# Performance work log

Hardware: AMD Instinct MI355X
Metric: run time of the kernel (lower is better)

## Reference

```python
import jax, jax.numpy as jnp
import numpy as np

GAMMA = 1.0

def setup_inputs() -> dict:
    key = jax.random.key(0)
    kx, ky = jax.random.split(key)
    X = jax.random.normal(kx, (8192, 64), dtype=jnp.float32)
    Y = jax.random.normal(ky, (8192, 64), dtype=jnp.float32)
    return {"X": X, "Y": Y}

def reference(X, Y):
    x2 = jnp.sum(X * X, axis=-1)            # (n,)
    y2 = jnp.sum(Y * Y, axis=-1)            # (m,)
    xy = X @ Y.T                            # (n, m)
    dist2 = x2[:, None] + y2[None, :] - 2.0 * xy
    dist2 = jnp.maximum(dist2, 0.0)         # numerical guard
    return jnp.exp(-GAMMA * dist2)
```

## Files before the change

### kernel.cpp

```cpp
#include <hip/hip_runtime.h>

typedef __attribute__((ext_vector_type(8))) short          short8_t;
typedef __attribute__((ext_vector_type(8))) unsigned short ushort8_t;
typedef __attribute__((ext_vector_type(4))) float          floatx4;

constexpr int N_ROWS = 8192;
constexpr int DIM    = 64;
constexpr int PANEL  = 128 * DIM;

__device__ __forceinline__ unsigned short bf16_rne(float f) {
    unsigned int u = __float_as_uint(f);
    u += 0x7FFFu + ((u >> 16) & 1u);
    return (unsigned short)(u >> 16);
}

__global__ void __launch_bounds__(256)
split_norms_kernel(const float* __restrict__ X, const float* __restrict__ Y,
                   float* __restrict__ x2n, float* __restrict__ y2n,
                   unsigned short* __restrict__ Xs, unsigned short* __restrict__ Ys) {
    const int t  = blockIdx.x * 256 + threadIdx.x;
    const int r  = t >> 1;
    const int h  = t & 1;
    const int p  = r >> 7;
    const int rl = r & 127;
    const int g  = rl >> 4;
    const int li = rl & 15;
    const size_t pb = (size_t)p * (2 * PANEL);

    const float4* xr = reinterpret_cast<const float4*>(X + (size_t)r * DIM + h * 32);
    const float4* yr = reinterpret_cast<const float4*>(Y + (size_t)r * DIM + h * 32);

    float sx = 0.f, sy = 0.f;
#pragma unroll
    for (int c = 0; c < 4; ++c) {
        const int off = ((g * 2 + h) * 64 + c * 16 + li) * 8;
        float f[8];
        ushort8_t hi, lo;

        *reinterpret_cast<float4*>(&f[0]) = xr[2 * c];
        *reinterpret_cast<float4*>(&f[4]) = xr[2 * c + 1];
#pragma unroll
        for (int e = 0; e < 8; ++e) {
            sx = fmaf(f[e], f[e], sx);
            unsigned short hh = bf16_rne(f[e]);
            hi[e] = hh;
            lo[e] = bf16_rne(f[e] - __uint_as_float((unsigned int)hh << 16));
        }
        *reinterpret_cast<ushort8_t*>(&Xs[pb + off])         = hi;
        *reinterpret_cast<ushort8_t*>(&Xs[pb + PANEL + off]) = lo;

        *reinterpret_cast<float4*>(&f[0]) = yr[2 * c];
        *reinterpret_cast<float4*>(&f[4]) = yr[2 * c + 1];
#pragma unroll
        for (int e = 0; e < 8; ++e) {
            sy = fmaf(f[e], f[e], sy);
            unsigned short hh = bf16_rne(f[e]);
            hi[e] = hh;
            lo[e] = bf16_rne(f[e] - __uint_as_float((unsigned int)hh << 16));
        }
        *reinterpret_cast<ushort8_t*>(&Ys[pb + off])         = hi;
        *reinterpret_cast<ushort8_t*>(&Ys[pb + PANEL + off]) = lo;
    }
    sx += __shfl_xor(sx, 1);
    sy += __shfl_xor(sy, 1);
    if (h == 0) { x2n[r] = -sx; y2n[r] = -sy; }
}

__global__ void __launch_bounds__(64)
rbf_mfma_kernel(const unsigned short* __restrict__ Xs,
                const unsigned short* __restrict__ Ys,
                const float* __restrict__ x2n, const float* __restrict__ y2n,
                float* __restrict__ out) {
    const int lane = threadIdx.x;
    const int row0 = blockIdx.y * 64;
    const int col0 = blockIdx.x * 64;
    const unsigned short* Xp = Xs + (size_t)(blockIdx.y >> 1) * (2 * PANEL);
    const unsigned short* Yp = Ys + (size_t)(blockIdx.x >> 1) * (2 * PANEL);
    const int gx0 = (blockIdx.y & 1) * 4;
    const int gy0 = (blockIdx.x & 1) * 4;

    floatx4 acc[4][4] = {};

#define GF(P, hl, g, ks)                                                       \
    (*reinterpret_cast<const short8_t*>(                                       \
        (P) + (hl) * PANEL + (((g) * 2 + (ks)) * 64 + lane) * 8))

#pragma unroll
    for (int ks = 0; ks < 2; ++ks) {
        short8_t aH[4], bH[4], aL[4], bL[4];
#pragma unroll
        for (int mi = 0; mi < 4; ++mi) aH[mi] = GF(Xp, 0, gx0 + mi, ks);
#pragma unroll
        for (int ni = 0; ni < 4; ++ni) bH[ni] = GF(Yp, 0, gy0 + ni, ks);
#pragma unroll
        for (int mi = 0; mi < 4; ++mi)
#pragma unroll
            for (int ni = 0; ni < 4; ++ni)
                acc[mi][ni] = __builtin_amdgcn_mfma_f32_16x16x32_bf16(
                    bH[ni], aH[mi], acc[mi][ni], 0, 0, 0);
#pragma unroll
        for (int ni = 0; ni < 4; ++ni) bL[ni] = GF(Yp, 1, gy0 + ni, ks);
#pragma unroll
        for (int mi = 0; mi < 4; ++mi)
#pragma unroll
            for (int ni = 0; ni < 4; ++ni)
                acc[mi][ni] = __builtin_amdgcn_mfma_f32_16x16x32_bf16(
                    bL[ni], aH[mi], acc[mi][ni], 0, 0, 0);
#pragma unroll
        for (int mi = 0; mi < 4; ++mi) aL[mi] = GF(Xp, 1, gx0 + mi, ks);
#pragma unroll
        for (int mi = 0; mi < 4; ++mi)
#pragma unroll
            for (int ni = 0; ni < 4; ++ni)
                acc[mi][ni] = __builtin_amdgcn_mfma_f32_16x16x32_bf16(
                    bH[ni], aL[mi], acc[mi][ni], 0, 0, 0);
    }
#undef GF

    const int li = lane & 15;
    const int lg = lane >> 4;
    const int orow = row0 + li;
    const int ocol = col0 + lg * 4;
#pragma unroll
    for (int mi = 0; mi < 4; ++mi) {
        const float xs = x2n[orow + mi * 16];
        float* obase = out + (size_t)(orow + mi * 16) * N_ROWS + ocol;
#pragma unroll
        for (int ni = 0; ni < 4; ++ni) {
            const float4 yv = *reinterpret_cast<const float4*>(&y2n[ocol + ni * 16]);
            floatx4 o;
            o[0] = __expf(fminf(fmaf(2.f, acc[mi][ni][0], xs + yv.x), 0.f));
            o[1] = __expf(fminf(fmaf(2.f, acc[mi][ni][1], xs + yv.y), 0.f));
            o[2] = __expf(fminf(fmaf(2.f, acc[mi][ni][2], xs + yv.z), 0.f));
            o[3] = __expf(fminf(fmaf(2.f, acc[mi][ni][3], xs + yv.w), 0.f));
            __builtin_nontemporal_store(o, reinterpret_cast<floatx4*>(obase + ni * 16));
        }
    }
}

extern "C" void kernel_launch(void* const* d_in, const int* in_sizes, int n_in,
                              void* d_out, int out_size, void* d_ws, size_t ws_size,
                              hipStream_t stream) {
    const float* X = (const float*)d_in[0];
    const float* Y = (const float*)d_in[1];
    float* out = (float*)d_out;

    float* x2n = (float*)d_ws;
    float* y2n = x2n + N_ROWS;
    unsigned short* Xs = (unsigned short*)(y2n + N_ROWS);
    unsigned short* Ys = Xs + (N_ROWS / 128) * 2 * PANEL;

    split_norms_kernel<<<(2 * N_ROWS) / 256, 256, 0, stream>>>(X, Y, x2n, y2n, Xs, Ys);

    dim3 grid(N_ROWS / 64, N_ROWS / 64);
    rbf_mfma_kernel<<<grid, 64, 0, stream>>>(Xs, Ys, x2n, y2n, out);
}
```

Measured before the change: 73.41 us.

## Stage Y strip in LDS via global_load_lds and keep X fragments in registers

Replaces the one-wave-per-64x64-tile grid with 256-thread blocks that each cover 256 rows by a 512-column strip. The strip's split-bf16 Y panels (128 KB) are copied into LDS once with direct global-to-LDS loads. Each wave keeps its X hi/lo fragments in registers and loops over eight 64-column chunks. This cuts redundant global operand loads and launch count, but the large LDS footprint limits occupancy to one block per CU and leaves little overlap between the initial LDS fill and compute.

```diff
diff --git a/kernel.cpp b/kernel.cpp
--- a/kernel.cpp
+++ b/kernel.cpp
@@ -7,11 +7,18 @@
 constexpr int N_ROWS = 8192;
 constexpr int DIM    = 64;
 constexpr int PANEL  = 128 * DIM;
+constexpr int STRIP  = 512;
 
 __device__ __forceinline__ unsigned short bf16_rne(float f) {
     unsigned int u = __float_as_uint(f);
     u += 0x7FFFu + ((u >> 16) & 1u);
     return (unsigned short)(u >> 16);
+}
+
+typedef __attribute__((address_space(1))) unsigned int gu32;
+typedef __attribute__((address_space(3))) unsigned int lu32;
+__device__ __forceinline__ void gload16(const void* g, void* l) {
+    __builtin_amdgcn_global_load_lds((gu32*)g, (lu32*)l, 16, 0, 0);
 }
 
 __global__ void __launch_bounds__(256)
@@ -66,74 +73,105 @@
     if (h == 0) { x2n[r] = -sx; y2n[r] = -sy; }
 }
 
-__global__ void __launch_bounds__(64)
+__global__ void __launch_bounds__(256)
 rbf_mfma_kernel(const unsigned short* __restrict__ Xs,
                 const unsigned short* __restrict__ Ys,
                 const float* __restrict__ x2n, const float* __restrict__ y2n,
                 float* __restrict__ out) {
-    const int lane = threadIdx.x;
-    const int row0 = blockIdx.y * 64;
-    const int col0 = blockIdx.x * 64;
-    const unsigned short* Xp = Xs + (size_t)(blockIdx.y >> 1) * (2 * PANEL);
-    const unsigned short* Yp = Ys + (size_t)(blockIdx.x >> 1) * (2 * PANEL);
-    const int gx0 = (blockIdx.y & 1) * 4;
-    const int gy0 = (blockIdx.x & 1) * 4;
+    extern __shared__ unsigned short Blds[];
 
-    floatx4 acc[4][4] = {};
+    const int tid  = threadIdx.x;
+    const int lane = tid & 63;
+    const int w    = tid >> 6;
+    const int strip = blockIdx.x;
+    const int band  = blockIdx.y;
 
-#define GF(P, hl, g, ks)                                                       \
-    (*reinterpret_cast<const short8_t*>(                                       \
-        (P) + (hl) * PANEL + (((g) * 2 + (ks)) * 64 + lane) * 8))
+    {
+        const unsigned short* src = Ys + (size_t)strip * (8 * PANEL);
+#pragma unroll
+        for (int it = 0; it < 32; ++it) {
+            const int ofs = ((w * 32 + it) * 64 + lane) * 8;
+            gload16(src + ofs, Blds + ofs);
+        }
+    }
 
+    const int row0 = band * 256 + w * 64;
+    short8_t aH[4][2], aL[4][2];
+    {
+        const int gx0 = row0 >> 4;
 #pragma unroll
-    for (int ks = 0; ks < 2; ++ks) {
-        short8_t aH[4], bH[4], aL[4], bL[4];
+        for (int gx = 0; gx < 4; ++gx) {
+            const int gabs = gx0 + gx;
+            const unsigned short* base = Xs + (size_t)(gabs >> 3) * (2 * PANEL);
+            const int g = gabs & 7;
 #pragma unroll
-        for (int mi = 0; mi < 4; ++mi) aH[mi] = GF(Xp, 0, gx0 + mi, ks);
-#pragma unroll
-        for (int ni = 0; ni < 4; ++ni) bH[ni] = GF(Yp, 0, gy0 + ni, ks);
-#pragma unroll
-        for (int mi = 0; mi < 4; ++mi)
-#pragma unroll
-            for (int ni = 0; ni < 4; ++ni)
-                acc[mi][ni] = __builtin_amdgcn_mfma_f32_16x16x32_bf16(
-                    bH[ni], aH[mi], acc[mi][ni], 0, 0, 0);
-#pragma unroll
-        for (int ni = 0; ni < 4; ++ni) bL[ni] = GF(Yp, 1, gy0 + ni, ks);
-#pragma unroll
-        for (int mi = 0; mi < 4; ++mi)
-#pragma unroll
-            for (int ni = 0; ni < 4; ++ni)
-                acc[mi][ni] = __builtin_amdgcn_mfma_f32_16x16x32_bf16(
-                    bL[ni], aH[mi], acc[mi][ni], 0, 0, 0);
-#pragma unroll
-        for (int mi = 0; mi < 4; ++mi) aL[mi] = GF(Xp, 1, gx0 + mi, ks);
-#pragma unroll
-        for (int mi = 0; mi < 4; ++mi)
-#pragma unroll
-            for (int ni = 0; ni < 4; ++ni)
-                acc[mi][ni] = __builtin_amdgcn_mfma_f32_16x16x32_bf16(
-                    bH[ni], aL[mi], acc[mi][ni], 0, 0, 0);
+            for (int ks = 0; ks < 2; ++ks) {
+                const int off = ((g * 2 + ks) * 64 + lane) * 8;
+                aH[gx][ks] = *reinterpret_cast<const short8_t*>(base + off);
+                aL[gx][ks] = *reinterpret_cast<const short8_t*>(base + PANEL + off);
+            }
+        }
     }
-#undef GF
+    __syncthreads();
 
     const int li = lane & 15;
     const int lg = lane >> 4;
-    const int orow = row0 + li;
-    const int ocol = col0 + lg * 4;
-#pragma unroll
-    for (int mi = 0; mi < 4; ++mi) {
-        const float xs = x2n[orow + mi * 16];
-        float* obase = out + (size_t)(orow + mi * 16) * N_ROWS + ocol;
+
+    for (int ch = 0; ch < 8; ++ch) {
+        short8_t bH[4][2], bL[4][2];
 #pragma unroll
         for (int ni = 0; ni < 4; ++ni) {
-            const float4 yv = *reinterpret_cast<const float4*>(&y2n[ocol + ni * 16]);
-            floatx4 o;
-            o[0] = __expf(fminf(fmaf(2.f, acc[mi][ni][0], xs + yv.x), 0.f));
-            o[1] = __expf(fminf(fmaf(2.f, acc[mi][ni][1], xs + yv.y), 0.f));
-            o[2] = __expf(fminf(fmaf(2.f, acc[mi][ni][2], xs + yv.z), 0.f));
-            o[3] = __expf(fminf(fmaf(2.f, acc[mi][ni][3], xs + yv.w), 0.f));
-            __builtin_nontemporal_store(o, reinterpret_cast<floatx4*>(obase + ni * 16));
+            const int gy = ch * 4 + ni;
+            const unsigned short* p =
+                Blds + (gy >> 3) * (2 * PANEL);
+            const int g = gy & 7;
+#pragma unroll
+            for (int ks = 0; ks < 2; ++ks) {
+                const int off = ((g * 2 + ks) * 64 + lane) * 8;
+                bH[ni][ks] = *reinterpret_cast<const short8_t*>(p + off);
+                bL[ni][ks] = *reinterpret_cast<const short8_t*>(p + PANEL + off);
+            }
+        }
+
+        floatx4 acc[4][4] = {};
+#pragma unroll
+        for (int ks = 0; ks < 2; ++ks) {
+#pragma unroll
+            for (int mi = 0; mi < 4; ++mi)
+#pragma unroll
+                for (int ni = 0; ni < 4; ++ni)
+                    acc[mi][ni] = __builtin_amdgcn_mfma_f32_16x16x32_bf16(
+                        bH[ni][ks], aH[mi][ks], acc[mi][ni], 0, 0, 0);
+#pragma unroll
+            for (int mi = 0; mi < 4; ++mi)
+#pragma unroll
+                for (int ni = 0; ni < 4; ++ni)
+                    acc[mi][ni] = __builtin_amdgcn_mfma_f32_16x16x32_bf16(
+                        bL[ni][ks], aH[mi][ks], acc[mi][ni], 0, 0, 0);
+#pragma unroll
+            for (int mi = 0; mi < 4; ++mi)
+#pragma unroll
+                for (int ni = 0; ni < 4; ++ni)
+                    acc[mi][ni] = __builtin_amdgcn_mfma_f32_16x16x32_bf16(
+                        bH[ni][ks], aL[mi][ks], acc[mi][ni], 0, 0, 0);
+        }
+
+        const int ocol = strip * STRIP + ch * 64 + lg * 4;
+#pragma unroll
+        for (int mi = 0; mi < 4; ++mi) {
+            const int rbase = row0 + mi * 16 + li;
+            const float xs = x2n[rbase];
+            float* obase = out + (size_t)rbase * N_ROWS + ocol;
+#pragma unroll
+            for (int ni = 0; ni < 4; ++ni) {
+                const float4 yv = *reinterpret_cast<const float4*>(&y2n[ocol + ni * 16]);
+                floatx4 o;
+                o[0] = __expf(fminf(fmaf(2.f, acc[mi][ni][0], xs + yv.x), 0.f));
+                o[1] = __expf(fminf(fmaf(2.f, acc[mi][ni][1], xs + yv.y), 0.f));
+                o[2] = __expf(fminf(fmaf(2.f, acc[mi][ni][2], xs + yv.z), 0.f));
+                o[3] = __expf(fminf(fmaf(2.f, acc[mi][ni][3], xs + yv.w), 0.f));
+                __builtin_nontemporal_store(o, reinterpret_cast<floatx4*>(obase + ni * 16));
+            }
         }
     }
 }
@@ -152,6 +190,6 @@
 
     split_norms_kernel<<<(2 * N_ROWS) / 256, 256, 0, stream>>>(X, Y, x2n, y2n, Xs, Ys);
 
-    dim3 grid(N_ROWS / 64, N_ROWS / 64);
-    rbf_mfma_kernel<<<grid, 64, 0, stream>>>(Xs, Ys, x2n, y2n, out);
+    dim3 grid(N_ROWS / STRIP, N_ROWS / 256);
+    rbf_mfma_kernel<<<grid, 256, 131072, stream>>>(Xs, Ys, x2n, y2n, out);
 }
```

After: 94.10 us. 28.2% more time.

## Fold norms into an extra MFMA k-step and remap blocks per XCD

Applied to the files above, without the earlier changes.

Pre-scales X by two and appends an extra K fragment holding bf16 hi/lo pieces of the negated norms and ones, so the MFMA accumulator directly yields the negated squared distance. This removes the per-element norm loads and FMAs from the epilogue. The kernel also moves to 256-thread blocks with four waves sharing one row tile, and uses an XCD-aware block-to-tile mapping to improve L2 reuse. The cost is one extra MFMA pass and a small bf16-split rounding error on the norms.

```diff
diff --git a/kernel.cpp b/kernel.cpp
--- a/kernel.cpp
+++ b/kernel.cpp
@@ -4,19 +4,23 @@
 typedef __attribute__((ext_vector_type(8))) unsigned short ushort8_t;
 typedef __attribute__((ext_vector_type(4))) float          floatx4;
 
-constexpr int N_ROWS = 8192;
-constexpr int DIM    = 64;
-constexpr int PANEL  = 128 * DIM;
+constexpr int N_ROWS  = 8192;
+constexpr int DIM     = 64;
+constexpr int PFRAG   = 128 * DIM;
+constexpr int PSTRIDE = 2 * PFRAG + 4096;
+constexpr unsigned short ONE_BF16 = 0x3F80;
 
 __device__ __forceinline__ unsigned short bf16_rne(float f) {
     unsigned int u = __float_as_uint(f);
     u += 0x7FFFu + ((u >> 16) & 1u);
     return (unsigned short)(u >> 16);
 }
+__device__ __forceinline__ float bf16_val(unsigned short h) {
+    return __uint_as_float((unsigned int)h << 16);
+}
 
 __global__ void __launch_bounds__(256)
 split_norms_kernel(const float* __restrict__ X, const float* __restrict__ Y,
-                   float* __restrict__ x2n, float* __restrict__ y2n,
                    unsigned short* __restrict__ Xs, unsigned short* __restrict__ Ys) {
     const int t  = blockIdx.x * 256 + threadIdx.x;
     const int r  = t >> 1;
@@ -25,7 +29,7 @@
     const int rl = r & 127;
     const int g  = rl >> 4;
     const int li = rl & 15;
-    const size_t pb = (size_t)p * (2 * PANEL);
+    const size_t pb = (size_t)p * PSTRIDE;
 
     const float4* xr = reinterpret_cast<const float4*>(X + (size_t)r * DIM + h * 32);
     const float4* yr = reinterpret_cast<const float4*>(Y + (size_t)r * DIM + h * 32);
@@ -42,12 +46,13 @@
 #pragma unroll
         for (int e = 0; e < 8; ++e) {
             sx = fmaf(f[e], f[e], sx);
-            unsigned short hh = bf16_rne(f[e]);
+            const float v2 = 2.f * f[e];
+            unsigned short hh = bf16_rne(v2);
             hi[e] = hh;
-            lo[e] = bf16_rne(f[e] - __uint_as_float((unsigned int)hh << 16));
+            lo[e] = bf16_rne(v2 - bf16_val(hh));
         }
         *reinterpret_cast<ushort8_t*>(&Xs[pb + off])         = hi;
-        *reinterpret_cast<ushort8_t*>(&Xs[pb + PANEL + off]) = lo;
+        *reinterpret_cast<ushort8_t*>(&Xs[pb + PFRAG + off]) = lo;
 
         *reinterpret_cast<float4*>(&f[0]) = yr[2 * c];
         *reinterpret_cast<float4*>(&f[4]) = yr[2 * c + 1];
@@ -56,34 +61,65 @@
             sy = fmaf(f[e], f[e], sy);
             unsigned short hh = bf16_rne(f[e]);
             hi[e] = hh;
-            lo[e] = bf16_rne(f[e] - __uint_as_float((unsigned int)hh << 16));
+            lo[e] = bf16_rne(f[e] - bf16_val(hh));
         }
         *reinterpret_cast<ushort8_t*>(&Ys[pb + off])         = hi;
-        *reinterpret_cast<ushort8_t*>(&Ys[pb + PANEL + off]) = lo;
+        *reinterpret_cast<ushort8_t*>(&Ys[pb + PFRAG + off]) = lo;
     }
     sx += __shfl_xor(sx, 1);
     sy += __shfl_xor(sy, 1);
-    if (h == 0) { x2n[r] = -sx; y2n[r] = -sy; }
-}
-
-__global__ void __launch_bounds__(64)
+
+    const int tb = 2 * PFRAG + g * 512;
+    ushort8_t zc = {0, 0, 0, 0, 0, 0, 0, 0};
+    if (h == 0) {
+        const unsigned short nx2h = bf16_rne(-sx);
+        const unsigned short nx2l = bf16_rne(-sx - bf16_val(nx2h));
+        const unsigned short ny2h = bf16_rne(-sy);
+        const unsigned short ny2l = bf16_rne(-sy - bf16_val(ny2h));
+        ushort8_t xt = {nx2h, nx2l, ONE_BF16, ONE_BF16, 0, 0, 0, 0};
+        ushort8_t yt = {ONE_BF16, ONE_BF16, ny2h, ny2l, 0, 0, 0, 0};
+        *reinterpret_cast<ushort8_t*>(&Xs[pb + tb + (0 * 16 + li) * 8]) = xt;
+        *reinterpret_cast<ushort8_t*>(&Ys[pb + tb + (0 * 16 + li) * 8]) = yt;
+        *reinterpret_cast<ushort8_t*>(&Xs[pb + tb + (1 * 16 + li) * 8]) = zc;
+        *reinterpret_cast<ushort8_t*>(&Ys[pb + tb + (1 * 16 + li) * 8]) = zc;
+    } else {
+        *reinterpret_cast<ushort8_t*>(&Xs[pb + tb + (2 * 16 + li) * 8]) = zc;
+        *reinterpret_cast<ushort8_t*>(&Ys[pb + tb + (2 * 16 + li) * 8]) = zc;
+        *reinterpret_cast<ushort8_t*>(&Xs[pb + tb + (3 * 16 + li) * 8]) = zc;
+        *reinterpret_cast<ushort8_t*>(&Ys[pb + tb + (3 * 16 + li) * 8]) = zc;
+    }
+}
+
+__global__ void __launch_bounds__(256)
 rbf_mfma_kernel(const unsigned short* __restrict__ Xs,
                 const unsigned short* __restrict__ Ys,
-                const float* __restrict__ x2n, const float* __restrict__ y2n,
                 float* __restrict__ out) {
-    const int lane = threadIdx.x;
-    const int row0 = blockIdx.y * 64;
-    const int col0 = blockIdx.x * 64;
-    const unsigned short* Xp = Xs + (size_t)(blockIdx.y >> 1) * (2 * PANEL);
-    const unsigned short* Yp = Ys + (size_t)(blockIdx.x >> 1) * (2 * PANEL);
-    const int gx0 = (blockIdx.y & 1) * 4;
-    const int gy0 = (blockIdx.x & 1) * 4;
+    const int tid  = threadIdx.x;
+    const int lane = tid & 63;
+    const int w    = tid >> 6;
+
+    const int bid   = blockIdx.x;
+    const int xcd   = bid & 7;
+    const int idx   = bid >> 3;
+    const int cquad = xcd * 4 + (idx >> 7);
+    const int rt    = idx & 127;
+
+    const int ct   = cquad * 4 + w;
+    const int row0 = rt * 64;
+    const int col0 = ct * 64;
+    const unsigned short* Xp = Xs + (size_t)(rt >> 1) * PSTRIDE;
+    const unsigned short* Yp = Ys + (size_t)(ct >> 1) * PSTRIDE;
+    const int gx0 = (rt & 1) * 4;
+    const int gy0 = (ct & 1) * 4;
 
     floatx4 acc[4][4] = {};
 
 #define GF(P, hl, g, ks)                                                       \
     (*reinterpret_cast<const short8_t*>(                                       \
-        (P) + (hl) * PANEL + (((g) * 2 + (ks)) * 64 + lane) * 8))
+        (P) + (hl) * PFRAG + (((g) * 2 + (ks)) * 64 + lane) * 8))
+#define GT(P, g)                                                               \
+    (*reinterpret_cast<const short8_t*>(                                       \
+        (P) + 2 * PFRAG + (g) * 512 + lane * 8))
 
 #pragma unroll
     for (int ks = 0; ks < 2; ++ks) {
@@ -115,24 +151,35 @@
                 acc[mi][ni] = __builtin_amdgcn_mfma_f32_16x16x32_bf16(
                     bH[ni], aL[mi], acc[mi][ni], 0, 0, 0);
     }
+    {
+        short8_t aT[4], bT[4];
+#pragma unroll
+        for (int mi = 0; mi < 4; ++mi) aT[mi] = GT(Xp, gx0 + mi);
+#pragma unroll
+        for (int ni = 0; ni < 4; ++ni) bT[ni] = GT(Yp, gy0 + ni);
+#pragma unroll
+        for (int mi = 0; mi < 4; ++mi)
+#pragma unroll
+            for (int ni = 0; ni < 4; ++ni)
+                acc[mi][ni] = __builtin_amdgcn_mfma_f32_16x16x32_bf16(
+                    bT[ni], aT[mi], acc[mi][ni], 0, 0, 0);
+    }
 #undef GF
+#undef GT
 
     const int li = lane & 15;
     const int lg = lane >> 4;
-    const int orow = row0 + li;
-    const int ocol = col0 + lg * 4;
 #pragma unroll
     for (int mi = 0; mi < 4; ++mi) {
-        const float xs = x2n[orow + mi * 16];
-        float* obase = out + (size_t)(orow + mi * 16) * N_ROWS + ocol;
+        const int row = row0 + mi * 16 + li;
+        float* obase = out + (size_t)row * N_ROWS + col0 + lg * 4;
 #pragma unroll
         for (int ni = 0; ni < 4; ++ni) {
-            const float4 yv = *reinterpret_cast<const float4*>(&y2n[ocol + ni * 16]);
             floatx4 o;
-            o[0] = __expf(fminf(fmaf(2.f, acc[mi][ni][0], xs + yv.x), 0.f));
-            o[1] = __expf(fminf(fmaf(2.f, acc[mi][ni][1], xs + yv.y), 0.f));
-            o[2] = __expf(fminf(fmaf(2.f, acc[mi][ni][2], xs + yv.z), 0.f));
-            o[3] = __expf(fminf(fmaf(2.f, acc[mi][ni][3], xs + yv.w), 0.f));
+            o[0] = __expf(fminf(acc[mi][ni][0], 0.f));
+            o[1] = __expf(fminf(acc[mi][ni][1], 0.f));
+            o[2] = __expf(fminf(acc[mi][ni][2], 0.f));
+            o[3] = __expf(fminf(acc[mi][ni][3], 0.f));
             __builtin_nontemporal_store(o, reinterpret_cast<floatx4*>(obase + ni * 16));
         }
     }
@@ -145,13 +192,10 @@
     const float* Y = (const float*)d_in[1];
     float* out = (float*)d_out;
 
-    float* x2n = (float*)d_ws;
-    float* y2n = x2n + N_ROWS;
-    unsigned short* Xs = (unsigned short*)(y2n + N_ROWS);
-    unsigned short* Ys = Xs + (N_ROWS / 128) * 2 * PANEL;
-
-    split_norms_kernel<<<(2 * N_ROWS) / 256, 256, 0, stream>>>(X, Y, x2n, y2n, Xs, Ys);
-
-    dim3 grid(N_ROWS / 64, N_ROWS / 64);
-    rbf_mfma_kernel<<<grid, 64, 0, stream>>>(Xs, Ys, x2n, y2n, out);
-}
+    unsigned short* Xs = (unsigned short*)d_ws;
+    unsigned short* Ys = Xs + (size_t)(N_ROWS / 128) * PSTRIDE;
+
+    split_norms_kernel<<<(2 * N_ROWS) / 256, 256, 0, stream>>>(X, Y, Xs, Ys);
+
+    rbf_mfma_kernel<<<4096, 256, 0, stream>>>(Xs, Ys, out);
+}
```

Result: slower. 118.3 us (+61.1%).
